# Performance work log

Hardware: AMD Instinct MI355X
Metric: run time of the kernel (lower is better)

The kernel has to match this reference:

```python
import jax, jax.numpy as jnp
import numpy as np

EPS = 1e-6

def ln(x):
    m = jnp.mean(x, axis=-1, keepdims=True)
    v = jnp.var(x, axis=-1, keepdims=True)
    return (x - m) * jax.lax.rsqrt(v + EPS)

def modulate(x, shift, scale):
    return x * (1.0 + scale[:, None, :]) + shift[:, None, :]

def setup_inputs() -> dict:
    key = jax.random.key(0)
    ks = jax.random.split(key, 16)
    B, N, H = 2, 384, 256
    D = 128  # n_vector_features * scale_dist_features
    MIN = 2 * H + D  # 640
    FH = 1024  # swiglu_correction_fn(4.0, 256)
    s = 0.02
    inp = {
        "mask": jnp.ones((B, N), jnp.float32),
        "x": jax.random.normal(ks[0], (B, N, H), jnp.float32),
        "t_emb": jax.random.normal(ks[1], (B, H), jnp.float32),
        "dist": jax.random.normal(ks[2], (B, N, N, D), jnp.float32),
        "edge_mask": jnp.ones((B, N, N), jnp.float32),
        "W_ada": jax.random.normal(ks[3], (6 * H, H), jnp.float32) * s,
        "b_ada": jnp.zeros((6 * H,), jnp.float32),
        "W_fe1": jax.random.normal(ks[4], (H, MIN), jnp.float32) * s,
        "b_fe1": jnp.zeros((H,), jnp.float32),
        "W_fe2": jax.random.normal(ks[5], (H, H), jnp.float32) * s,
        "b_fe2": jnp.zeros((H,), jnp.float32),
        "W_qkv": jax.random.normal(ks[6], (3 * H, H), jnp.float32) * s,
        "W_out": jax.random.normal(ks[7], (H, H), jnp.float32) * s,
        "W_ffn1": jax.random.normal(ks[8], (2 * FH, H), jnp.float32) * s,
        "W_ffn2": jax.random.normal(ks[9], (H, FH), jnp.float32) * s,
    }
    return inp

def reference(mask, x, t_emb, dist, edge_mask, W_ada, b_ada, W_fe1, b_fe1,
              W_fe2, b_fe2, W_qkv, W_out, W_ffn1, W_ffn2):
    B, N, H = x.shape
    num_heads = 8
    d_head = H // num_heads
    mN = mask[..., None]  # (B,N,1)

    # adaLN modulation
    ada = jax.nn.silu(t_emb) @ W_ada.T + b_ada  # (B,6H)
    shift_msa, scale_msa, gate_msa, shift_mlp, scale_mlp, gate_mlp = jnp.split(ada, 6, axis=1)

    x_norm = modulate(ln(x * mN), shift_msa, scale_msa)  # (B,N,H)

    # all-pairs message passing: concat(h_i, h_j, dist_ij) -> MLP -> sum_j
    h1 = jnp.broadcast_to(x_norm[:, :, None, :], (B, N, N, H))
    h2 = jnp.broadcast_to(x_norm[:, None, :, :], (B, N, N, H))
    feats = jnp.concatenate([h1, h2, dist], axis=-1) * edge_mask[..., None]
    msgs = jax.nn.silu(feats @ W_fe1.T + b_fe1) @ W_fe2.T + b_fe2  # (B,N,N,H)
    x_msg = jnp.sum(msgs, axis=-2)  # (B,N,H)

    # attention
    qkv = x_msg @ W_qkv.T
    Q, K, V = jnp.split(qkv, 3, axis=-1)
    Q = ln(Q * mN)
    K = ln(K * mN)
    def heads(t):
        return t.reshape(B, N, num_heads, d_head).transpose(0, 2, 1, 3)  # b h s d
    Q, K, V = heads(Q), heads(K), heads(V)
    scores = jnp.einsum("bhqd,bhkd->bhqk", Q, K) / jnp.sqrt(jnp.float32(d_head))
    bias = jnp.where(mask[:, None, None, :] > 0, 0.0, -1e9)
    attn = jax.nn.softmax(scores + bias, axis=-1)
    ao = jnp.einsum("bhqk,bhkd->bhqd", attn, V)
    ao = ao.transpose(0, 2, 1, 3).reshape(B, N, H)
    y = ao @ W_out.T

    x = x + gate_msa[:, None, :] * y

    # SwiGLU FFN
    xm = modulate(ln(x * mN), shift_mlp, scale_mlp)
    h12 = xm @ W_ffn1.T
    h_a, h_b = jnp.split(h12, 2, axis=-1)
    ffn_out = (jax.nn.silu(h_a) * h_b) @ W_ffn2.T
    x = (x + gate_mlp[:, None, :] * ffn_out) * mN
    return x
```

## Files before the change

kernel.cpp:

```cpp
#include <hip/hip_runtime.h>

#define DEVI __device__ __forceinline__

typedef float fv4 __attribute__((ext_vector_type(4)));
typedef __bf16 bf16x8 __attribute__((ext_vector_type(8)));
typedef unsigned short u16x8 __attribute__((ext_vector_type(8)));
typedef unsigned short u16x4 __attribute__((ext_vector_type(4)));

DEVI fv4 ldv4(const float* p) { return *reinterpret_cast<const fv4*>(p); }
DEVI bf16x8 pkbf(fv4 a, fv4 b) {
  bf16x8 r;
  r[0] = (__bf16)a[0]; r[1] = (__bf16)a[1]; r[2] = (__bf16)a[2]; r[3] = (__bf16)a[3];
  r[4] = (__bf16)b[0]; r[5] = (__bf16)b[1]; r[6] = (__bf16)b[2]; r[7] = (__bf16)b[3];
  return r;
}
DEVI u16x8 b2u(bf16x8 v) { return __builtin_bit_cast(u16x8, v); }
DEVI bf16x8 asbf(u16x8 u) { return __builtin_bit_cast(bf16x8, u); }
DEVI unsigned short bfbits(float x) { __bf16 v = (__bf16)x; return __builtin_bit_cast(unsigned short, v); }
DEVI u16x4 pk4(fv4 a) {
  u16x4 u;
  u[0] = bfbits(a[0]); u[1] = bfbits(a[1]); u[2] = bfbits(a[2]); u[3] = bfbits(a[3]);
  return u;
}
DEVI fv4 MFMA16(bf16x8 a, bf16x8 b, fv4 c) {
  return __builtin_amdgcn_mfma_f32_16x16x32_bf16(a, b, c, 0, 0, 0);
}
DEVI float siluf(float x) {
  float e = __builtin_amdgcn_exp2f(x * -1.44269504f);
  return x * __builtin_amdgcn_rcpf(1.f + e);
}
DEVI fv4 glu4(fv4 x, fv4 y) {
  fv4 r;
#pragma unroll
  for (int j = 0; j < 4; ++j) r[j] = siluf(x[j]) * y[j];
  return r;
}
DEVI int swz(int row, int k) {
  int unit = k >> 3;
  int phys = (unit & ~7) | ((unit ^ row) & 7);
  return row * 384 + (phys << 3) + (k & 7);
}

__global__ __launch_bounds__(256)
void k_ada(const float* __restrict__ temb, const float* __restrict__ W_ada,
           const float* __restrict__ b_ada, float* __restrict__ ada) {
  __shared__ float sm[256];
  const int b = blockIdx.x / 6;
  const int r = (blockIdx.x % 6) * 256 + threadIdx.x;
  sm[threadIdx.x] = siluf(temb[b * 256 + threadIdx.x]);
  __syncthreads();
  float s = b_ada[r];
  const float* wr = W_ada + (size_t)r * 256;
  for (int k = 0; k < 256; ++k) s += sm[k] * wr[k];
  ada[b * 1536 + r] = s;
}

__global__ __launch_bounds__(256)
void k_xnorm(const float* __restrict__ xin, const float* __restrict__ mask,
             const float* __restrict__ ada, int shift_off, int scale_off,
             float* __restrict__ out) {
  const int row = blockIdx.x;
  const int b = row / 384;
  const int t = threadIdx.x;
  const float m = mask[row];
  const float v = xin[(size_t)row * 256 + t] * m;
  float s = v, ss = v * v;
#pragma unroll
  for (int o = 1; o < 64; o <<= 1) { s += __shfl_xor(s, o); ss += __shfl_xor(ss, o); }
  __shared__ float red[8];
  const int wid = t >> 6;
  if ((t & 63) == 0) { red[wid] = s; red[4 + wid] = ss; }
  __syncthreads();
  s = red[0] + red[1] + red[2] + red[3];
  ss = red[4] + red[5] + red[6] + red[7];
  const float mean = s * (1.f / 256.f);
  const float var = ss * (1.f / 256.f) - mean * mean;
  const float rs = rsqrtf(var + 1e-6f);
  out[(size_t)row * 256 + t] =
      (v - mean) * rs * (1.f + ada[b * 1536 + scale_off + t]) + ada[b * 1536 + shift_off + t];
}

template <int EPI, int AMODE>
__global__ __launch_bounds__(256)
void k_gemm(const float* __restrict__ A, int lda,
            const float* __restrict__ B, int ldb, int koff, int K,
            float* __restrict__ C, int ldc,
            const float* __restrict__ bias, float bscale,
            const float* __restrict__ res,
            const float* __restrict__ ada, int gate_off,
            const float* __restrict__ mask) {
  __shared__ __align__(16) unsigned short As[64 * 64];
  __shared__ __align__(16) unsigned short Bs[64 * 64];
  const int t = threadIdx.x, lane = t & 63, w = t >> 6;
  const int bn0 = blockIdx.x * 64, bm0 = blockIdx.y * 64;
  const int qr = (w >> 1) * 32, qc = (w & 1) * 32;
  const int g = lane >> 4, c = lane & 15;
  const int srow = t >> 2;
  const int so = (t & 3) * 2;
  const int o0 = so ^ (srow & 7), o1 = (so + 1) ^ (srow & 7);
  unsigned short* aw0 = As + srow * 64 + o0 * 8;
  unsigned short* aw1 = As + srow * 64 + o1 * 8;
  unsigned short* bw0 = Bs + srow * 64 + o0 * 8;
  unsigned short* bw1 = Bs + srow * 64 + o1 * 8;
  const float* ag = A + (size_t)(bm0 + srow) * lda + so * 8;
  const float* bg = B + (size_t)(bn0 + srow) * ldb + koff + so * 8;
  const float* a2g = nullptr;
  if constexpr (AMODE == 2) a2g = res + ((size_t)(bm0 + srow) * lda + so * 8);
  fv4 a0 = ldv4(ag), a1 = ldv4(ag + 4), a2 = ldv4(ag + 8), a3 = ldv4(ag + 12);
  fv4 x0, x1, x2, x3;
  if constexpr (AMODE == 1) {
    x0 = ldv4(ag + 1024); x1 = ldv4(ag + 1028); x2 = ldv4(ag + 1032); x3 = ldv4(ag + 1036);
  }
  if constexpr (AMODE == 2) {
    x0 = ldv4(a2g); x1 = ldv4(a2g + 4); x2 = ldv4(a2g + 8); x3 = ldv4(a2g + 12);
  }
  fv4 c0 = ldv4(bg), c1 = ldv4(bg + 4), c2 = ldv4(bg + 8), c3 = ldv4(bg + 12);
  fv4 acc[2][2] = {};
  for (int k0 = 0; k0 < K; k0 += 64) {
    __syncthreads();
    if constexpr (AMODE == 1) {
      *reinterpret_cast<u16x8*>(aw0) = b2u(pkbf(glu4(a0, x0), glu4(a1, x1)));
      *reinterpret_cast<u16x8*>(aw1) = b2u(pkbf(glu4(a2, x2), glu4(a3, x3)));
    } else if constexpr (AMODE == 2) {
      *reinterpret_cast<u16x8*>(aw0) = b2u(pkbf(a0 + x0, a1 + x1));
      *reinterpret_cast<u16x8*>(aw1) = b2u(pkbf(a2 + x2, a3 + x3));
    } else {
      *reinterpret_cast<u16x8*>(aw0) = b2u(pkbf(a0, a1));
      *reinterpret_cast<u16x8*>(aw1) = b2u(pkbf(a2, a3));
    }
    *reinterpret_cast<u16x8*>(bw0) = b2u(pkbf(c0, c1));
    *reinterpret_cast<u16x8*>(bw1) = b2u(pkbf(c2, c3));
    __syncthreads();
    if (k0 + 64 < K) {
      ag += 64; bg += 64;
      a0 = ldv4(ag); a1 = ldv4(ag + 4); a2 = ldv4(ag + 8); a3 = ldv4(ag + 12);
      if constexpr (AMODE == 1) {
        x0 = ldv4(ag + 1024); x1 = ldv4(ag + 1028); x2 = ldv4(ag + 1032); x3 = ldv4(ag + 1036);
      }
      if constexpr (AMODE == 2) {
        a2g += 64;
        x0 = ldv4(a2g); x1 = ldv4(a2g + 4); x2 = ldv4(a2g + 8); x3 = ldv4(a2g + 12);
      }
      c0 = ldv4(bg); c1 = ldv4(bg + 4); c2 = ldv4(bg + 8); c3 = ldv4(bg + 12);
    }
#pragma unroll
    for (int kk = 0; kk < 2; ++kk) {
      bf16x8 af[2], bf[2];
#pragma unroll
      for (int mi = 0; mi < 2; ++mi) {
        int row = qr + mi * 16 + c;
        int oct = (kk * 4 + g) ^ (row & 7);
        af[mi] = asbf(*reinterpret_cast<const u16x8*>(As + row * 64 + oct * 8));
      }
#pragma unroll
      for (int ni = 0; ni < 2; ++ni) {
        int row = qc + ni * 16 + c;
        int oct = (kk * 4 + g) ^ (row & 7);
        bf[ni] = asbf(*reinterpret_cast<const u16x8*>(Bs + row * 64 + oct * 8));
      }
#pragma unroll
      for (int mi = 0; mi < 2; ++mi)
#pragma unroll
        for (int ni = 0; ni < 2; ++ni)
          acc[mi][ni] = MFMA16(af[mi], bf[ni], acc[mi][ni]);
    }
  }
#pragma unroll
  for (int mi = 0; mi < 2; ++mi)
#pragma unroll
    for (int ni = 0; ni < 2; ++ni)
#pragma unroll
      for (int r = 0; r < 4; ++r) {
        int row = bm0 + qr + mi * 16 + g * 4 + r;
        int col = bn0 + qc + ni * 16 + c;
        float v = acc[mi][ni][r];
        if constexpr (EPI == 1) v += bscale * bias[col];
        if constexpr (EPI == 2) v = res[(size_t)row * 256 + col] + ada[(row / 384) * 1536 + gate_off + col] * v;
        if constexpr (EPI == 3) v = (res[(size_t)row * 256 + col] + ada[(row / 384) * 1536 + gate_off + col] * v) * mask[row];
        if constexpr (EPI == 5) C[(((size_t)(row >> 4) * 256 + col) << 4) + (row & 15)] = v;
        else C[(size_t)row * ldc + col] = v;
      }
}

__global__ __launch_bounds__(256)
void k_edge(const float* __restrict__ dist, const float* __restrict__ emask,
            const float* __restrict__ Wfe1, const float* __restrict__ bfe1,
            const float* __restrict__ P, const float* __restrict__ Qc,
            float* __restrict__ S0, float* __restrict__ S1) {
  const int blk = blockIdx.x;
  const int jh = blockIdx.y;
  const int b = blk / 384, i = blk - b * 384;
  const int t = threadIdx.x, lane = t & 63, w = t >> 6;
  const int g = lane >> 4, c = lane & 15;
  const int l5 = lane >> 5, l31 = lane & 31;
  __shared__ __align__(16) unsigned short Al[2][4][16 * 136];

  bf16x8 Bf[4][4];
#pragma unroll
  for (int ht = 0; ht < 4; ++ht) {
    const int h = w * 64 + ht * 16 + c;
    const float* wp = Wfe1 + (size_t)h * 640 + 512 + g * 8;
#pragma unroll
    for (int ks = 0; ks < 4; ++ks)
      Bf[ht][ks] = pkbf(ldv4(wp + ks * 32), ldv4(wp + ks * 32 + 4));
  }
  float Pl[4], bl[4];
#pragma unroll
  for (int ht = 0; ht < 4; ++ht) {
    int h = w * 64 + ht * 16 + c;
    Pl[ht] = P[(size_t)(b * 384 + i) * 256 + h];
    bl[ht] = bfe1[h];
  }
  float Ss[4] = {0.f, 0.f, 0.f, 0.f};

  const float* dbase = dist + (size_t)(b * 384 + i) * 49152 + (size_t)jh * 24576;
  const float* embase = emask + (size_t)(b * 384 + i) * 384 + jh * 192;

  fv4 dreg[8];
#pragma unroll
  for (int tt = 0; tt < 8; ++tt) dreg[tt] = ldv4(dbase + tt * 256 + lane * 4);
#pragma unroll
  for (int tt = 0; tt < 8; ++tt) {
    int row = tt * 2 + l5;
    *reinterpret_cast<u16x4*>(&Al[0][w][row * 136 + l31 * 4]) = pk4(dreg[tt]);
  }
  for (int cl = 0; cl < 12; ++cl) {
    fv4 emv = ldv4(embase + cl * 16 + g * 4);
    const int jc = b * 24 + jh * 12 + cl;
    fv4 qv[4];
#pragma unroll
    for (int ht = 0; ht < 4; ++ht) {
      int h = w * 64 + ht * 16 + c;
      qv[ht] = ldv4(Qc + (((size_t)jc * 256 + h) << 4) + g * 4);
    }
    if (cl < 11) {
      const float* dg = dbase + (size_t)(cl + 1) * 2048 + lane * 4;
#pragma unroll
      for (int tt = 0; tt < 8; ++tt) dreg[tt] = ldv4(dg + tt * 256);
    }
    const unsigned short* rb = &Al[cl & 1][w][0];
    fv4 acc[4] = {};
#pragma unroll
    for (int ks = 0; ks < 4; ++ks) {
      bf16x8 af = asbf(*reinterpret_cast<const u16x8*>(rb + c * 136 + ks * 32 + g * 8));
#pragma unroll
      for (int ht = 0; ht < 4; ++ht)
        acc[ht] = MFMA16(af, Bf[ht][ks], acc[ht]);
    }
#pragma unroll
    for (int ht = 0; ht < 4; ++ht)
#pragma unroll
      for (int r = 0; r < 4; ++r)
        Ss[ht] += siluf(emv[r] * (acc[ht][r] + Pl[ht] + qv[ht][r]) + bl[ht]);
    if (cl < 11) {
      unsigned short* wb = &Al[(cl + 1) & 1][w][0];
#pragma unroll
      for (int tt = 0; tt < 8; ++tt) {
        int row = tt * 2 + l5;
        *reinterpret_cast<u16x4*>(&wb[row * 136 + l31 * 4]) = pk4(dreg[tt]);
      }
    }
  }
  float* Sp = jh ? S1 : S0;
#pragma unroll
  for (int ht = 0; ht < 4; ++ht) {
    float s = Ss[ht];
    s += __shfl_xor(s, 16);
    s += __shfl_xor(s, 32);
    if (g == 0) Sp[(size_t)(b * 384 + i) * 256 + w * 64 + ht * 16 + c] = s;
  }
}

__global__ __launch_bounds__(256)
void k_lnqk(const float* __restrict__ qkv, const float* __restrict__ mask,
            float* __restrict__ Qn, float* __restrict__ Kn) {
  const int row = blockIdx.x, t = threadIdx.x;
  const float m = mask[row];
  const float q = qkv[(size_t)row * 768 + t] * m;
  const float k = qkv[(size_t)row * 768 + 256 + t] * m;
  float sq = q, sqq = q * q, sk = k, skk = k * k;
#pragma unroll
  for (int o = 1; o < 64; o <<= 1) {
    sq += __shfl_xor(sq, o); sqq += __shfl_xor(sqq, o);
    sk += __shfl_xor(sk, o); skk += __shfl_xor(skk, o);
  }
  __shared__ float red[16];
  const int wid = t >> 6;
  if ((t & 63) == 0) { red[wid] = sq; red[4 + wid] = sqq; red[8 + wid] = sk; red[12 + wid] = skk; }
  __syncthreads();
  sq = red[0] + red[1] + red[2] + red[3];
  sqq = red[4] + red[5] + red[6] + red[7];
  sk = red[8] + red[9] + red[10] + red[11];
  skk = red[12] + red[13] + red[14] + red[15];
  const float mq = sq * (1.f / 256.f), vq = sqq * (1.f / 256.f) - mq * mq;
  const float mk = sk * (1.f / 256.f), vk = skk * (1.f / 256.f) - mk * mk;
  Qn[(size_t)row * 256 + t] = (q - mq) * rsqrtf(vq + 1e-6f);
  Kn[(size_t)row * 256 + t] = (k - mk) * rsqrtf(vk + 1e-6f);
}

__global__ __launch_bounds__(256)
void k_attn(const float* __restrict__ Qn, const float* __restrict__ Kn,
            const float* __restrict__ qkv, const float* __restrict__ mask,
            float* __restrict__ ao) {
  const int bh = blockIdx.y, b = bh >> 3, h = bh & 7;
  const int qg = blockIdx.x;
  const int t = threadIdx.x, lane = t & 63, w = t >> 6;
  const int g = lane >> 4, c = lane & 15;
  __shared__ __align__(16) unsigned short Vt[32 * 384];
  __shared__ __align__(16) unsigned short pl[16 * 384];
  __shared__ float outp[4][16][32];
  __shared__ float redm[4][16], reds[4][16];

  {
    const int d0 = (t & 7) * 4;
    const int kp = t >> 3;
#pragma unroll
    for (int pass = 0; pass < 6; ++pass) {
      int k = pass * 64 + kp * 2;
      fv4 v0 = ldv4(qkv + (size_t)(b * 384 + k) * 768 + 512 + h * 32 + d0);
      fv4 v1 = ldv4(qkv + (size_t)(b * 384 + k + 1) * 768 + 512 + h * 32 + d0);
#pragma unroll
      for (int j = 0; j < 4; ++j) {
        int d = d0 + j;
        unsigned int pr = (unsigned int)bfbits(v0[j]) | ((unsigned int)bfbits(v1[j]) << 16);
        *reinterpret_cast<unsigned int*>(&Vt[swz(d, k)]) = pr;
      }
    }
  }
  bf16x8 qf;
  {
    const float* qp = Qn + (size_t)(b * 384 + qg * 16 + c) * 256 + h * 32 + g * 8;
    qf = pkbf(ldv4(qp), ldv4(qp + 4));
  }
  fv4 sc[6];
#pragma unroll
  for (int kb = 0; kb < 6; ++kb) {
    const float* kp2 = Kn + (size_t)(b * 384 + w * 96 + kb * 16 + c) * 256 + h * 32 + g * 8;
    bf16x8 kf = pkbf(ldv4(kp2), ldv4(kp2 + 4));
    fv4 z = {0.f, 0.f, 0.f, 0.f};
    sc[kb] = MFMA16(qf, kf, z);
  }
  const float rs = 0.1767766952966369f;
  float zz[6][4], mx[4] = {-3e38f, -3e38f, -3e38f, -3e38f};
#pragma unroll
  for (int kb = 0; kb < 6; ++kb) {
    float mb = mask[b * 384 + w * 96 + kb * 16 + c] > 0.f ? 0.f : -1e9f;
#pragma unroll
    for (int r = 0; r < 4; ++r) {
      zz[kb][r] = sc[kb][r] * rs + mb;
      mx[r] = fmaxf(mx[r], zz[kb][r]);
    }
  }
#pragma unroll
  for (int r = 0; r < 4; ++r) {
#pragma unroll
    for (int o = 1; o < 16; o <<= 1) mx[r] = fmaxf(mx[r], __shfl_xor(mx[r], o));
  }
  if (c == 0) {
#pragma unroll
    for (int r = 0; r < 4; ++r) redm[w][g * 4 + r] = mx[r];
  }
  __syncthreads();
  float m4[4], sm[4] = {0.f, 0.f, 0.f, 0.f};
#pragma unroll
  for (int r = 0; r < 4; ++r) {
    int q = g * 4 + r;
    m4[r] = fmaxf(fmaxf(redm[0][q], redm[1][q]), fmaxf(redm[2][q], redm[3][q]));
  }
#pragma unroll
  for (int kb = 0; kb < 6; ++kb) {
    int k = w * 96 + kb * 16 + c;
#pragma unroll
    for (int r = 0; r < 4; ++r) {
      float p = __builtin_amdgcn_exp2f((zz[kb][r] - m4[r]) * 1.44269504f);
      sm[r] += p;
      pl[swz(g * 4 + r, k)] = bfbits(p);
    }
  }
#pragma unroll
  for (int r = 0; r < 4; ++r) {
#pragma unroll
    for (int o = 1; o < 16; o <<= 1) sm[r] += __shfl_xor(sm[r], o);
  }
  if (c == 0) {
#pragma unroll
    for (int r = 0; r < 4; ++r) reds[w][g * 4 + r] = sm[r];
  }
  __syncthreads();
  fv4 oacc[2] = {};
#pragma unroll
  for (int kk = 0; kk < 3; ++kk) {
    int kbase = w * 96 + kk * 32 + g * 8;
    bf16x8 pa = asbf(*reinterpret_cast<const u16x8*>(&pl[swz(c, kbase)]));
#pragma unroll
    for (int db = 0; db < 2; ++db) {
      int d = db * 16 + c;
      bf16x8 vb = asbf(*reinterpret_cast<const u16x8*>(&Vt[swz(d, kbase)]));
      oacc[db] = MFMA16(pa, vb, oacc[db]);
    }
  }
#pragma unroll
  for (int db = 0; db < 2; ++db)
#pragma unroll
    for (int r = 0; r < 4; ++r) outp[w][g * 4 + r][db * 16 + c] = oacc[db][r];
  __syncthreads();
#pragma unroll
  for (int idx = t; idx < 512; idx += 256) {
    int q = idx >> 5, d = idx & 31;
    float v = outp[0][q][d] + outp[1][q][d] + outp[2][q][d] + outp[3][q][d];
    float s = reds[0][q] + reds[1][q] + reds[2][q] + reds[3][q];
    ao[(size_t)(b * 384 + qg * 16 + q) * 256 + h * 32 + d] = v / s;
  }
}

extern "C" void kernel_launch(void* const* d_in, const int* in_sizes, int n_in,
                              void* d_out, int out_size, void* d_ws, size_t ws_size,
                              hipStream_t stream) {
  (void)in_sizes; (void)n_in; (void)out_size; (void)ws_size;
  const float* mask   = (const float*)d_in[0];
  const float* x      = (const float*)d_in[1];
  const float* temb   = (const float*)d_in[2];
  const float* dist   = (const float*)d_in[3];
  const float* emask  = (const float*)d_in[4];
  const float* W_ada  = (const float*)d_in[5];
  const float* b_ada  = (const float*)d_in[6];
  const float* W_fe1  = (const float*)d_in[7];
  const float* b_fe1  = (const float*)d_in[8];
  const float* W_fe2  = (const float*)d_in[9];
  const float* b_fe2  = (const float*)d_in[10];
  const float* W_qkv  = (const float*)d_in[11];
  const float* W_out  = (const float*)d_in[12];
  const float* W_ffn1 = (const float*)d_in[13];
  const float* W_ffn2 = (const float*)d_in[14];
  float* out = (float*)d_out;
  float* ws = (float*)d_ws;

  float* ada   = ws;
  float* xattn = ws + 4096;
  float* xm    = ws + 200704;
  float* xn    = ws + 397312;
  float* P     = ws + 593920;
  float* Qc    = ws + 790528;
  float* S0    = ws + 987136;
  float* xmsg  = ws + 1183744;
  float* qkvb  = ws + 1380352;
  float* Qn    = ws + 1970176;
  float* Kn    = ws + 2166784;
  float* aob   = ws + 2363392;
  float* S1    = ws + 2363392;
  float* h12   = ws + 397312;

  k_ada<<<12, 256, 0, stream>>>(temb, W_ada, b_ada, ada);
  k_xnorm<<<768, 256, 0, stream>>>(x, mask, ada, 0, 256, xn);
  k_gemm<0, 0><<<dim3(4, 12), 256, 0, stream>>>(xn, 256, W_fe1, 640, 0, 256, P, 256,
                                                nullptr, 0.f, nullptr, nullptr, 0, nullptr);
  k_gemm<5, 0><<<dim3(4, 12), 256, 0, stream>>>(xn, 256, W_fe1, 640, 256, 256, Qc, 0,
                                                nullptr, 0.f, nullptr, nullptr, 0, nullptr);
  k_edge<<<dim3(768, 2), 256, 0, stream>>>(dist, emask, W_fe1, b_fe1, P, Qc, S0, S1);
  k_gemm<1, 2><<<dim3(4, 12), 256, 0, stream>>>(S0, 256, W_fe2, 256, 0, 256, xmsg, 256,
                                                b_fe2, 384.f, S1, nullptr, 0, nullptr);
  k_gemm<0, 0><<<dim3(12, 12), 256, 0, stream>>>(xmsg, 256, W_qkv, 256, 0, 256, qkvb, 768,
                                                 nullptr, 0.f, nullptr, nullptr, 0, nullptr);
  k_lnqk<<<768, 256, 0, stream>>>(qkvb, mask, Qn, Kn);
  k_attn<<<dim3(24, 16), 256, 0, stream>>>(Qn, Kn, qkvb, mask, aob);
  k_gemm<2, 0><<<dim3(4, 12), 256, 0, stream>>>(aob, 256, W_out, 256, 0, 256, xattn, 256,
                                                nullptr, 0.f, x, ada, 512, nullptr);
  k_xnorm<<<768, 256, 0, stream>>>(xattn, mask, ada, 768, 1024, xm);
  k_gemm<0, 0><<<dim3(32, 12), 256, 0, stream>>>(xm, 256, W_ffn1, 256, 0, 256, h12, 2048,
                                                 nullptr, 0.f, nullptr, nullptr, 0, nullptr);
  k_gemm<3, 1><<<dim3(4, 12), 256, 0, stream>>>(h12, 2048, W_ffn2, 1024, 0, 1024, out, 256,
                                                nullptr, 0.f, xattn, ada, 1280, mask);
}
```

Before: 166.0 us.

## Share dist tile across 8 waves in edge kernel with swizzled LDS double buffer

After: 149.6 us. 9.9% less time.

```diff
diff --git a/kernel.cpp b/kernel.cpp
--- a/kernel.cpp
+++ b/kernel.cpp
@@ -182,92 +182,116 @@
       }
 }
 
-__global__ __launch_bounds__(256)
+__global__ __launch_bounds__(512)
 void k_edge(const float* __restrict__ dist, const float* __restrict__ emask,
             const float* __restrict__ Wfe1, const float* __restrict__ bfe1,
             const float* __restrict__ P, const float* __restrict__ Qc,
             float* __restrict__ S0, float* __restrict__ S1) {
-  const int blk = blockIdx.x;
-  const int jh = blockIdx.y;
+  const int blk = blockIdx.x, jh = blockIdx.y;
   const int b = blk / 384, i = blk - b * 384;
   const int t = threadIdx.x, lane = t & 63, w = t >> 6;
   const int g = lane >> 4, c = lane & 15;
-  const int l5 = lane >> 5, l31 = lane & 31;
-  __shared__ __align__(16) unsigned short Al[2][4][16 * 136];
-
-  bf16x8 Bf[4][4];
-#pragma unroll
-  for (int ht = 0; ht < 4; ++ht) {
-    const int h = w * 64 + ht * 16 + c;
+  __shared__ __align__(16) unsigned short Al[2][16 * 128];
+
+  bf16x8 Bf[2][4];
+  float Pl[2], bl[2], Ss[2] = {0.f, 0.f};
+#pragma unroll
+  for (int ht = 0; ht < 2; ++ht) {
+    const int h = w * 32 + ht * 16 + c;
     const float* wp = Wfe1 + (size_t)h * 640 + 512 + g * 8;
 #pragma unroll
     for (int ks = 0; ks < 4; ++ks)
       Bf[ht][ks] = pkbf(ldv4(wp + ks * 32), ldv4(wp + ks * 32 + 4));
-  }
-  float Pl[4], bl[4];
-#pragma unroll
-  for (int ht = 0; ht < 4; ++ht) {
-    int h = w * 64 + ht * 16 + c;
     Pl[ht] = P[(size_t)(b * 384 + i) * 256 + h];
     bl[ht] = bfe1[h];
   }
-  float Ss[4] = {0.f, 0.f, 0.f, 0.f};
-
   const float* dbase = dist + (size_t)(b * 384 + i) * 49152 + (size_t)jh * 24576;
   const float* embase = emask + (size_t)(b * 384 + i) * 384 + jh * 192;
-
-  fv4 dreg[8];
-#pragma unroll
-  for (int tt = 0; tt < 8; ++tt) dreg[tt] = ldv4(dbase + tt * 256 + lane * 4);
-#pragma unroll
-  for (int tt = 0; tt < 8; ++tt) {
-    int row = tt * 2 + l5;
-    *reinterpret_cast<u16x4*>(&Al[0][w][row * 136 + l31 * 4]) = pk4(dreg[tt]);
-  }
-  for (int cl = 0; cl < 12; ++cl) {
-    fv4 emv = ldv4(embase + cl * 16 + g * 4);
-    const int jc = b * 24 + jh * 12 + cl;
-    fv4 qv[4];
-#pragma unroll
-    for (int ht = 0; ht < 4; ++ht) {
-      int h = w * 64 + ht * 16 + c;
-      qv[ht] = ldv4(Qc + (((size_t)jc * 256 + h) << 4) + g * 4);
-    }
-    if (cl < 11) {
-      const float* dg = dbase + (size_t)(cl + 1) * 2048 + lane * 4;
-#pragma unroll
-      for (int tt = 0; tt < 8; ++tt) dreg[tt] = ldv4(dg + tt * 256);
-    }
-    const unsigned short* rb = &Al[cl & 1][w][0];
-    fv4 acc[4] = {};
-#pragma unroll
-    for (int ks = 0; ks < 4; ++ks) {
-      bf16x8 af = asbf(*reinterpret_cast<const u16x8*>(rb + c * 136 + ks * 32 + g * 8));
-#pragma unroll
-      for (int ht = 0; ht < 4; ++ht)
-        acc[ht] = MFMA16(af, Bf[ht][ks], acc[ht]);
-    }
-#pragma unroll
-    for (int ht = 0; ht < 4; ++ht)
-#pragma unroll
-      for (int r = 0; r < 4; ++r)
-        Ss[ht] += siluf(emv[r] * (acc[ht][r] + Pl[ht] + qv[ht][r]) + bl[ht]);
-    if (cl < 11) {
-      unsigned short* wb = &Al[(cl + 1) & 1][w][0];
-#pragma unroll
-      for (int tt = 0; tt < 8; ++tt) {
-        int row = tt * 2 + l5;
-        *reinterpret_cast<u16x4*>(&wb[row * 136 + l31 * 4]) = pk4(dreg[tt]);
-      }
+  const int jcb = b * 24 + jh * 12;
+  const int h0 = w * 32 + c, h1 = h0 + 16;
+
+  const int srow = t >> 5, kq = t & 31;
+  const int sunit = kq >> 1;
+  const int sphys = (sunit & 8) | ((sunit ^ (srow & 7)) & 7);
+  const int soff = srow * 128 + sphys * 8 + (kq & 1) * 4;
+
+  fv4 rX, rY, qvX0, qvX1, qvY0, qvY1, emX, emY;
+  {
+    fv4 t0 = ldv4(dbase + t * 4);
+    *reinterpret_cast<u16x4*>(&Al[0][soff]) = pk4(t0);
+  }
+  rX = ldv4(dbase + 2048 + t * 4);
+  qvX0 = ldv4(Qc + (((size_t)jcb * 256 + h0) << 4) + g * 4);
+  qvX1 = ldv4(Qc + (((size_t)jcb * 256 + h1) << 4) + g * 4);
+  emX = ldv4(embase + g * 4);
+  __syncthreads();
+
+#pragma unroll 1
+  for (int p = 0; p < 6; ++p) {
+    {
+      const int cl = 2 * p;
+      if (cl <= 9) rY = ldv4(dbase + (size_t)(cl + 2) * 2048 + t * 4);
+      if (cl <= 10) {
+        *reinterpret_cast<u16x4*>(&Al[1][soff]) = pk4(rX);
+        const size_t jc = (size_t)(jcb + cl + 1);
+        qvY0 = ldv4(Qc + ((jc * 256 + h0) << 4) + g * 4);
+        qvY1 = ldv4(Qc + ((jc * 256 + h1) << 4) + g * 4);
+        emY = ldv4(embase + (cl + 1) * 16 + g * 4);
+      }
+      fv4 acc0, acc1;
+#pragma unroll
+      for (int r = 0; r < 4; ++r) { acc0[r] = Pl[0] + qvX0[r]; acc1[r] = Pl[1] + qvX1[r]; }
+#pragma unroll
+      for (int ks = 0; ks < 4; ++ks) {
+        const int u = ks * 4 + g;
+        const int phys = (u & 8) | ((u ^ (c & 7)) & 7);
+        bf16x8 af = asbf(*reinterpret_cast<const u16x8*>(&Al[0][c * 128 + phys * 8]));
+        acc0 = MFMA16(af, Bf[0][ks], acc0);
+        acc1 = MFMA16(af, Bf[1][ks], acc1);
+      }
+#pragma unroll
+      for (int r = 0; r < 4; ++r) {
+        Ss[0] += siluf(emX[r] * acc0[r] + bl[0]);
+        Ss[1] += siluf(emX[r] * acc1[r] + bl[1]);
+      }
+      __syncthreads();
+    }
+    {
+      const int cl = 2 * p + 1;
+      if (cl <= 9) rX = ldv4(dbase + (size_t)(cl + 2) * 2048 + t * 4);
+      if (cl <= 10) {
+        *reinterpret_cast<u16x4*>(&Al[0][soff]) = pk4(rY);
+        const size_t jc = (size_t)(jcb + cl + 1);
+        qvX0 = ldv4(Qc + ((jc * 256 + h0) << 4) + g * 4);
+        qvX1 = ldv4(Qc + ((jc * 256 + h1) << 4) + g * 4);
+        emX = ldv4(embase + (cl + 1) * 16 + g * 4);
+      }
+      fv4 acc0, acc1;
+#pragma unroll
+      for (int r = 0; r < 4; ++r) { acc0[r] = Pl[0] + qvY0[r]; acc1[r] = Pl[1] + qvY1[r]; }
+#pragma unroll
+      for (int ks = 0; ks < 4; ++ks) {
+        const int u = ks * 4 + g;
+        const int phys = (u & 8) | ((u ^ (c & 7)) & 7);
+        bf16x8 af = asbf(*reinterpret_cast<const u16x8*>(&Al[1][c * 128 + phys * 8]));
+        acc0 = MFMA16(af, Bf[0][ks], acc0);
+        acc1 = MFMA16(af, Bf[1][ks], acc1);
+      }
+#pragma unroll
+      for (int r = 0; r < 4; ++r) {
+        Ss[0] += siluf(emY[r] * acc0[r] + bl[0]);
+        Ss[1] += siluf(emY[r] * acc1[r] + bl[1]);
+      }
+      __syncthreads();
     }
   }
   float* Sp = jh ? S1 : S0;
 #pragma unroll
-  for (int ht = 0; ht < 4; ++ht) {
+  for (int ht = 0; ht < 2; ++ht) {
     float s = Ss[ht];
     s += __shfl_xor(s, 16);
     s += __shfl_xor(s, 32);
-    if (g == 0) Sp[(size_t)(b * 384 + i) * 256 + w * 64 + ht * 16 + c] = s;
+    if (g == 0) Sp[(size_t)(b * 384 + i) * 256 + w * 32 + ht * 16 + c] = s;
   }
 }
 
@@ -456,7 +480,7 @@
                                                 nullptr, 0.f, nullptr, nullptr, 0, nullptr);
   k_gemm<5, 0><<<dim3(4, 12), 256, 0, stream>>>(xn, 256, W_fe1, 640, 256, 256, Qc, 0,
                                                 nullptr, 0.f, nullptr, nullptr, 0, nullptr);
-  k_edge<<<dim3(768, 2), 256, 0, stream>>>(dist, emask, W_fe1, b_fe1, P, Qc, S0, S1);
+  k_edge<<<dim3(768, 2), 512, 0, stream>>>(dist, emask, W_fe1, b_fe1, P, Qc, S0, S1);
   k_gemm<1, 2><<<dim3(4, 12), 256, 0, stream>>>(S0, 256, W_fe2, 256, 0, 256, xmsg, 256,
                                                 b_fe2, 384.f, S1, nullptr, 0, nullptr);
   k_gemm<0, 0><<<dim3(12, 12), 256, 0, stream>>>(xmsg, 256, W_qkv, 256, 0, 256, qkvb, 768,
```
